# Kernel tuning notes

Hardware: AMD Instinct MI355X
Metric: run time of the kernel (lower is better)

The kernel has to match this reference:

```python
import jax, jax.numpy as jnp
import numpy as np
from jax import lax

B, N, NP, NS, CIN = 4, 8192, 2048, 32, 64
RADIUS = 0.1
CH = [CIN + 3, 64, 64, 128]  # mlp[0] += 3 because use_xyz=True
EPS = 1e-5


def _gather(x, idx):
    # x: [B, N, D], idx: [B, ...] int -> [B, ..., D]
    return jax.vmap(lambda a, i: a[i])(x, idx)


def _fps(xyz, npoint):
    # furthest point sampling, returns indices [B, npoint]
    b, n, _ = xyz.shape
    init_idx = jnp.zeros((b,), jnp.int32)
    dist0 = jnp.full((b, n), 1e10, xyz.dtype)

    def body(carry, _):
        dist, last = carry
        p = jnp.take_along_axis(xyz, last[:, None, None], axis=1)  # [B,1,3]
        d = jnp.sum((xyz - p) ** 2, axis=-1)                       # [B,N]
        dist = jnp.minimum(dist, d)
        nxt = jnp.argmax(dist, axis=-1).astype(jnp.int32)
        return (dist, nxt), nxt

    (_, _), rest = lax.scan(body, (dist0, init_idx), None, length=npoint - 1)
    return jnp.concatenate([init_idx[None, :], rest], axis=0).T    # [B, npoint]


def _ball_query(xyz, new_xyz, radius, nsample):
    # first `nsample` points within radius; pad with the first hit (0 if none)
    n = xyz.shape[1]
    d2 = jnp.sum((new_xyz[:, :, None, :] - xyz[:, None, :, :]) ** 2, axis=-1)  # [B,NP,N]
    score = jnp.where(d2 < radius * radius, jnp.arange(n, dtype=jnp.int32), n)
    neg_vals, _ = lax.top_k(-score, nsample)   # smallest indices first
    idx = -neg_vals                            # [B,NP,nsample]
    first = idx[..., :1]
    fill = jnp.where(first >= n, 0, first)
    return jnp.where(idx >= n, fill, idx)


def setup_inputs() -> dict:
    key = jax.random.key(0)
    ks = jax.random.split(key, 16)
    inp = {
        "xyz": jax.random.uniform(ks[0], (B, N, 3), jnp.float32),
        "features": jax.random.normal(ks[1], (B, CIN, N), jnp.float32),
    }
    for i in range(3):
        ci, co = CH[i], CH[i + 1]
        inp[f"W{i}"] = jax.random.normal(ks[2 + 4 * i], (co, ci), jnp.float32) / np.sqrt(ci)
        inp[f"b{i}"] = jnp.zeros((co,), jnp.float32)
        inp[f"g{i}"] = jnp.ones((co,), jnp.float32)
        inp[f"beta{i}"] = jnp.zeros((co,), jnp.float32)
    return inp


def _forward(xyz, features, params):
    fps_idx = _fps(xyz, NP)
    new_xyz = _gather(xyz, fps_idx)                                 # [B,NP,3]
    idx = _ball_query(xyz, new_xyz, RADIUS, NS)                     # [B,NP,NS]
    g_xyz = _gather(xyz, idx) - new_xyz[:, :, None, :]              # relative xyz
    g_feat = _gather(jnp.swapaxes(features, 1, 2), idx)             # [B,NP,NS,CIN]
    h = jnp.concatenate([g_xyz, g_feat], axis=-1)                   # [B,NP,NS,3+CIN]
    for (W, b, g, be) in params:
        h = jnp.einsum('bpsc,oc->bpso', h, W) + b                   # 1x1 conv
        mu = jnp.mean(h, axis=(0, 1, 2))
        var = jnp.var(h, axis=(0, 1, 2))
        h = (h - mu) * lax.rsqrt(var + EPS) * g + be                # BatchNorm2d (batch stats)
        h = jax.nn.relu(h)
    new_features = jnp.max(h, axis=2)                               # max-pool over nsample
    return new_xyz, jnp.swapaxes(new_features, 1, 2)                # [B,Cout,NP]


def reference(xyz, features, W0, b0, g0, beta0, W1, b1, g1, beta1, W2, b2, g2, beta2):
    params = ((W0, b0, g0, beta0), (W1, b1, g1, beta1), (W2, b2, g2, beta2))
    return _forward(xyz, features, params)
```

## Files before the change

### kernel.cpp

```cpp
#include <hip/hip_runtime.h>
#include <hip/hip_bf16.h>
#include <cstdint>

#define B_   4
#define N_   8192
#define NP_  2048
#define NS_  32
#define CIN_ 64
#define M_   (B_*NP_*NS_)
#define EPS_ 1e-5f
#define R2_  0.01f

typedef unsigned long long ull;
typedef float v2f __attribute__((ext_vector_type(2)));

__global__ __launch_bounds__(256) void transpose_kernel(const float* __restrict__ feat,
                                                        __hip_bfloat16* __restrict__ featT)
{
    __shared__ float tile[64][65];
    const int b  = blockIdx.y;
    const int j0 = blockIdx.x * 64;
    const int tx = threadIdx.x & 63, ty = threadIdx.x >> 6;
    for (int cc = ty; cc < 64; cc += 4)
        tile[tx][cc] = feat[((size_t)(b*CIN_ + cc))*N_ + j0 + tx];
    __syncthreads();
    for (int cc = ty; cc < 64; cc += 4)
        featT[((size_t)(b*N_ + j0 + cc))*64 + tx] = __float2bfloat16(tile[cc][tx]);
}

template<int CTRL>
__device__ __forceinline__ float dppmaxf(float v)
{
    int o = __builtin_amdgcn_update_dpp(__float_as_int(v), __float_as_int(v), CTRL, 0xF, 0xF, false);
    return fmaxf(v, __int_as_float(o));
}

__global__ __launch_bounds__(512) void fps_kernel(const float* __restrict__ xyz,
    int* __restrict__ fps_idx, float* __restrict__ new_xyzf, float* __restrict__ out)
{
#pragma clang fp contract(off)
    const int b = blockIdx.x;
    const int t = threadIdx.x;
    const float* X = xyz + (size_t)b * N_ * 3;

    __shared__ float xs[N_], ys[N_], zs[N_];
    __shared__ float wavemax[8];
    __shared__ unsigned widx_slot[2];

    for (int p = t; p < N_; p += 512) {
        xs[p] = X[p*3+0]; ys[p] = X[p*3+1]; zs[p] = X[p*3+2];
    }
    if (t < 2) widx_slot[t] = 0u;

    v2f px[8], py[8], pz[8], dst[8];
#pragma unroll
    for (int g = 0; g < 8; ++g) {
        const int p0 = (2*g)*512 + t, p1 = (2*g+1)*512 + t;
        px[g] = (v2f){X[p0*3+0], X[p1*3+0]};
        py[g] = (v2f){X[p0*3+1], X[p1*3+1]};
        pz[g] = (v2f){X[p0*3+2], X[p1*3+2]};
        dst[g] = (v2f){1e10f, 1e10f};
    }
    const int wv = t >> 6, ln = t & 63;

    float cx = X[0], cy = X[1], cz = X[2];
    if (t == 0) {
        fps_idx[b*NP_] = 0;
        size_t o3 = (size_t)(b*NP_) * 3;
        new_xyzf[o3] = cx; new_xyzf[o3+1] = cy; new_xyzf[o3+2] = cz;
        out[o3] = cx; out[o3+1] = cy; out[o3+2] = cz;
    }
    for (int it = 1; it < NP_; ++it) {
        const int par = it & 1;
        float bestv = -1.0f;
        const v2f c0 = (v2f){cx, cx}, c1 = (v2f){cy, cy}, c2 = (v2f){cz, cz};
#pragma unroll
        for (int g = 0; g < 8; ++g) {
            v2f dx = px[g] - c0, dy = py[g] - c1, dz = pz[g] - c2;
            v2f dd = dx*dx;
            dd = dd + dy*dy;
            dd = dd + dz*dz;
            v2f nd;
            nd.x = fminf(dst[g].x, dd.x);
            nd.y = fminf(dst[g].y, dd.y);
            dst[g] = nd;
            bestv = fmaxf(bestv, nd.x);
            bestv = fmaxf(bestv, nd.y);
        }
        float wm = bestv;
        wm = dppmaxf<0x111>(wm);
        wm = dppmaxf<0x112>(wm);
        wm = dppmaxf<0x114>(wm);
        wm = dppmaxf<0x118>(wm);
        wm = dppmaxf<0x142>(wm);
        wm = dppmaxf<0x143>(wm);
        if (ln == 63) wavemax[wv] = wm;
        __syncthreads();
        if (t == 0) widx_slot[par ^ 1] = 0u;
        float bmax = fmaxf(fmaxf(fmaxf(wavemax[0], wavemax[1]), fmaxf(wavemax[2], wavemax[3])),
                           fmaxf(fmaxf(wavemax[4], wavemax[5]), fmaxf(wavemax[6], wavemax[7])));
        if (bestv == bmax) {
            unsigned nin = 0u;
#pragma unroll
            for (int g = 7; g >= 0; --g) {
                if (dst[g].y == bmax) nin = ~(unsigned)((2*g+1)*512 + t);
                if (dst[g].x == bmax) nin = ~(unsigned)((2*g)*512 + t);
            }
            atomicMax(&widx_slot[par], nin);
        }
        __syncthreads();
        const int widx = (int)(~widx_slot[par]);
        cx = xs[widx]; cy = ys[widx]; cz = zs[widx];
        if (t == 0) {
            fps_idx[b*NP_ + it] = widx;
            size_t o3 = ((size_t)(b*NP_ + it)) * 3;
            new_xyzf[o3] = cx; new_xyzf[o3+1] = cy; new_xyzf[o3+2] = cz;
            out[o3] = cx; out[o3+1] = cy; out[o3+2] = cz;
        }
    }
}

__global__ __launch_bounds__(256) void ball_kernel(const float* __restrict__ xyz,
    const float* __restrict__ new_xyzf, int* __restrict__ ballidx)
{
#pragma clang fp contract(off)
    const int gw   = (blockIdx.x * 256 + threadIdx.x) >> 6;
    const int lane = threadIdx.x & 63;
    const int b    = gw >> 11;
    const float* X = xyz + (size_t)b * N_ * 3;
    const float cx = new_xyzf[(size_t)gw*3];
    const float cy = new_xyzf[(size_t)gw*3+1];
    const float cz = new_xyzf[(size_t)gw*3+2];
    int* outp = ballidx + (size_t)gw * NS_;
    int total = 0, first = -1;
    for (int base = 0; base < N_; base += 64) {
        const int j = base + lane;
        float dx = cx - X[j*3], dy = cy - X[j*3+1], dz = cz - X[j*3+2];
        float d2 = dx*dx;
        d2 = d2 + dy*dy;
        d2 = d2 + dz*dz;
        const bool in = d2 <= R2_;
        ull m = __ballot(in);
        if (m) {
            if (first < 0) first = base + __builtin_ctzll(m);
            int r = total + __popcll(m & ((1ull << lane) - 1ull));
            if (in && r < NS_) outp[r] = j;
            total += (int)__popcll(m);
            if (total >= NS_) break;
        }
    }
    if (total < NS_) {
        int f = first < 0 ? 0 : first;
        if (lane >= total && lane < NS_) outp[lane] = f;
    }
}

__global__ __launch_bounds__(256) void gemm1_kernel(const float* __restrict__ xyz,
    const __hip_bfloat16* __restrict__ featT, const float* __restrict__ newxyz,
    const int* __restrict__ ballidx, const float* __restrict__ W, const float* __restrict__ bias,
    __hip_bfloat16* __restrict__ pre1, float* __restrict__ psum, float* __restrict__ psumsq)
{
    const int lane = threadIdx.x & 63;
    const int gw   = (blockIdx.x * 256 + threadIdx.x) >> 6;
    float w[67];
#pragma unroll
    for (int k = 0; k < 67; ++k) w[k] = W[lane*67 + k];
    const float bs = bias[lane];
    float s1 = 0.f, s2 = 0.f;
    for (int r = gw; r < M_; r += 4096) {
        const int b = r >> 16;
        const int p = (r & 65535) >> 5;
        const int j = ballidx[r];
        const float* xp = xyz    + ((size_t)b*N_  + j)*3;
        const float* cp = newxyz + ((size_t)b*NP_ + p)*3;
        float acc = bs;
        acc = fmaf(xp[0] - cp[0], w[0], acc);
        acc = fmaf(xp[1] - cp[1], w[1], acc);
        acc = fmaf(xp[2] - cp[2], w[2], acc);
        const unsigned* rp = (const unsigned*)(featT + ((size_t)b*N_ + j)*64);
#pragma unroll
        for (int kk = 0; kk < 32; ++kk) {
            unsigned u = rp[kk];
            float v0 = __uint_as_float(u << 16);
            float v1 = __uint_as_float(u & 0xffff0000u);
            acc = fmaf(v0, w[3 + 2*kk], acc);
            acc = fmaf(v1, w[4 + 2*kk], acc);
        }
        pre1[(size_t)r*64 + lane] = __float2bfloat16(acc);
        s1 += acc;
        s2 = fmaf(acc, acc, s2);
    }
    psum  [(size_t)gw*64 + lane] = s1;
    psumsq[(size_t)gw*64 + lane] = s2;
}

__global__ __launch_bounds__(256) void gemm2_kernel(__hip_bfloat16* __restrict__ buf,
    const float* __restrict__ W, const float* __restrict__ bias,
    const float* __restrict__ bnsc, const float* __restrict__ bnsh,
    float* __restrict__ psum, float* __restrict__ psumsq)
{
    const int lane = threadIdx.x & 63;
    const int gw   = (blockIdx.x * 256 + threadIdx.x) >> 6;
    __shared__ float ssc[64], ssh[64];
    if (threadIdx.x < 64) { ssc[threadIdx.x] = bnsc[threadIdx.x]; ssh[threadIdx.x] = bnsh[threadIdx.x]; }
    __syncthreads();
    float w[64];
#pragma unroll
    for (int k = 0; k < 64; ++k) w[k] = W[lane*64 + k];
    const float bs = bias[lane];
    float s1 = 0.f, s2 = 0.f;
    for (int r = gw; r < M_; r += 4096) {
        const unsigned* rp = (const unsigned*)(buf + (size_t)r*64);
        float acc = bs;
#pragma unroll
        for (int kk = 0; kk < 32; ++kk) {
            unsigned u = rp[kk];
            float v0 = __uint_as_float(u << 16);
            float v1 = __uint_as_float(u & 0xffff0000u);
            v0 = fmaxf(fmaf(v0, ssc[2*kk],   ssh[2*kk]),   0.f);
            v1 = fmaxf(fmaf(v1, ssc[2*kk+1], ssh[2*kk+1]), 0.f);
            acc = fmaf(v0, w[2*kk],   acc);
            acc = fmaf(v1, w[2*kk+1], acc);
        }
        buf[(size_t)r*64 + lane] = __float2bfloat16(acc);
        s1 += acc;
        s2 = fmaf(acc, acc, s2);
    }
    psum  [(size_t)gw*64 + lane] = s1;
    psumsq[(size_t)gw*64 + lane] = s2;
}

__global__ __launch_bounds__(256) void gemm3_kernel(const __hip_bfloat16* __restrict__ pre2,
    const float* __restrict__ W, const float* __restrict__ bias,
    const float* __restrict__ bnsc, const float* __restrict__ bnsh,
    float* __restrict__ mxb, float* __restrict__ mnb,
    float* __restrict__ psum, float* __restrict__ psumsq)
{
    const int lane = threadIdx.x & 63;
    const int gw   = (blockIdx.x * 256 + threadIdx.x) >> 6;
    const int pt   = gw >> 1;
    const int half = gw & 1;
    __shared__ float ssc[64], ssh[64];
    if (threadIdx.x < 64) { ssc[threadIdx.x] = bnsc[threadIdx.x]; ssh[threadIdx.x] = bnsh[threadIdx.x]; }
    __syncthreads();
    const int o = half*64 + lane;
    float w[64];
#pragma unroll
    for (int k = 0; k < 64; ++k) w[k] = W[o*64 + k];
    const float bs = bias[o];
    float s1 = 0.f, s2 = 0.f, mx = -1e30f, mn = 1e30f;
    for (int s = 0; s < NS_; ++s) {
        const size_t r = (size_t)pt*NS_ + s;
        const unsigned* rp = (const unsigned*)(pre2 + r*64);
        float acc = bs;
#pragma unroll
        for (int kk = 0; kk < 32; ++kk) {
            unsigned u = rp[kk];
            float v0 = __uint_as_float(u << 16);
            float v1 = __uint_as_float(u & 0xffff0000u);
            v0 = fmaxf(fmaf(v0, ssc[2*kk],   ssh[2*kk]),   0.f);
            v1 = fmaxf(fmaf(v1, ssc[2*kk+1], ssh[2*kk+1]), 0.f);
            acc = fmaf(v0, w[2*kk],   acc);
            acc = fmaf(v1, w[2*kk+1], acc);
        }
        s1 += acc;
        s2 = fmaf(acc, acc, s2);
        mx = fmaxf(mx, acc);
        mn = fminf(mn, acc);
    }
    mxb[(size_t)pt*128 + o] = mx;
    mnb[(size_t)pt*128 + o] = mn;
    psum  [(size_t)pt*128 + o] = s1;
    psumsq[(size_t)pt*128 + o] = s2;
}

template<int CO>
__global__ __launch_bounds__(256) void bnred_kernel(const float* __restrict__ psum,
    const float* __restrict__ psumsq, const float* __restrict__ g, const float* __restrict__ beta,
    float* __restrict__ sc, float* __restrict__ sh, int nslots)
{
    const int c = blockIdx.x;
    const int t = threadIdx.x;
    float s1 = 0, s2 = 0;
    for (int i = t; i < nslots; i += 256) {
        s1 += psum  [(size_t)i*CO + c];
        s2 += psumsq[(size_t)i*CO + c];
    }
    __shared__ float a1[256], a2[256];
    a1[t] = s1; a2[t] = s2;
    __syncthreads();
    for (int st = 128; st > 0; st >>= 1) {
        if (t < st) { a1[t] += a1[t+st]; a2[t] += a2[t+st]; }
        __syncthreads();
    }
    if (t == 0) {
        const float invM = 1.0f / (float)M_;
        float mu  = a1[0] * invM;
        float var = fmaxf(a2[0] * invM - mu*mu, 0.f);
        float rs  = 1.0f / sqrtf(var + EPS_);
        float s   = rs * g[c];
        sc[c] = s;
        sh[c] = fmaf(-mu, s, beta[c]);
    }
}

__global__ __launch_bounds__(256) void final_kernel(const float* __restrict__ mxb,
    const float* __restrict__ mnb, const float* __restrict__ sc, const float* __restrict__ sh,
    float* __restrict__ out)
{
    __shared__ float tile[128][65];
    const int b = blockIdx.y, p0 = blockIdx.x * 64;
    {
        const int o = threadIdx.x & 127, ph = threadIdx.x >> 7;
        const float s = sc[o], h = sh[o];
        const bool pos = (s >= 0.f);
        for (int pl = ph; pl < 64; pl += 2) {
            const size_t pt = (size_t)b*NP_ + p0 + pl;
            float v = pos ? mxb[pt*128 + o] : mnb[pt*128 + o];
            tile[o][pl] = fmaxf(fmaf(v, s, h), 0.f);
        }
    }
    __syncthreads();
    {
        const int p = threadIdx.x & 63, oh = threadIdx.x >> 6;
        for (int oo = oh; oo < 128; oo += 4)
            out[(size_t)(B_*NP_*3) + ((size_t)(b*128 + oo))*NP_ + p0 + p] = tile[oo][p];
    }
}

extern "C" void kernel_launch(void* const* d_in, const int* in_sizes, int n_in,
                              void* d_out, int out_size, void* d_ws, size_t ws_size,
                              hipStream_t stream)
{
    const float* xyz  = (const float*)d_in[0];
    const float* feat = (const float*)d_in[1];
    const float* W0   = (const float*)d_in[2];
    const float* b0   = (const float*)d_in[3];
    const float* g0   = (const float*)d_in[4];
    const float* be0  = (const float*)d_in[5];
    const float* W1   = (const float*)d_in[6];
    const float* b1   = (const float*)d_in[7];
    const float* g1   = (const float*)d_in[8];
    const float* be1  = (const float*)d_in[9];
    const float* W2   = (const float*)d_in[10];
    const float* b2   = (const float*)d_in[11];
    const float* g2   = (const float*)d_in[12];
    const float* be2  = (const float*)d_in[13];

    char* ws = (char*)d_ws;
    int*   fpsidx = (int*)  (ws + 0);
    float* newxyz = (float*)(ws + 32768);
    int*   ball   = (int*)  (ws + 131072);
    float* scb    = (float*)(ws + 1179648);
    float* psum   = (float*)(ws + 1183744);
    float* psumsq = (float*)(ws + 5378048);
    __hip_bfloat16* featT = (__hip_bfloat16*)(ws + 9572352);
    float* mxb    = (float*)(ws + 13766656);
    float* mnb    = (float*)(ws + 17960960);
    __hip_bfloat16* buf1 = (__hip_bfloat16*)(ws + 22155264);
    float* out = (float*)d_out;

    float* sc1 = scb;       float* sh1 = scb + 128;
    float* sc2 = scb + 256; float* sh2 = scb + 384;
    float* sc3 = scb + 512; float* sh3 = scb + 640;

    transpose_kernel<<<dim3(N_/64, B_), 256, 0, stream>>>(feat, featT);
    fps_kernel<<<dim3(B_), 512, 0, stream>>>(xyz, fpsidx, newxyz, out);
    ball_kernel<<<dim3(B_*NP_/4), 256, 0, stream>>>(xyz, newxyz, ball);

    gemm1_kernel<<<1024, 256, 0, stream>>>(xyz, featT, newxyz, ball, W0, b0, buf1, psum, psumsq);
    bnred_kernel<64><<<64, 256, 0, stream>>>(psum, psumsq, g0, be0, sc1, sh1, 4096);
    gemm2_kernel<<<1024, 256, 0, stream>>>(buf1, W1, b1, sc1, sh1, psum, psumsq);
    bnred_kernel<64><<<64, 256, 0, stream>>>(psum, psumsq, g1, be1, sc2, sh2, 4096);
    gemm3_kernel<<<4096, 256, 0, stream>>>(buf1, W2, b2, sc2, sh2, mxb, mnb, psum, psumsq);
    bnred_kernel<128><<<128, 256, 0, stream>>>(psum, psumsq, g2, be2, sc3, sh3, 8192);
    final_kernel<<<dim3(NP_/64, B_), 256, 0, stream>>>(mxb, mnb, sc3, sh3, out);
}
```

Baseline: 2.545 ms.

## Pick FPS winner via wave ballot and pass coordinates through shared slot

Each thread now owns a contiguous block of 16 points instead of a 512-strided set. With that layout, the lowest-index winner is found by taking the lowest wave whose maximum matches, then the lowest lane in a ballot, with no shared-memory atomicMax. The winning thread writes its own register coordinates into a small shared slot. This removes the 96KB shared xyz copy and the atomic. The risk is that the contiguous per-thread layout makes the initial global loads uncoalesced, though those run only once.

Result: slower. 2.790 ms (+9.7%).

```diff
diff --git a/kernel.cpp b/kernel.cpp
--- a/kernel.cpp
+++ b/kernel.cpp
@@ -43,19 +43,14 @@
     const int t = threadIdx.x;
     const float* X = xyz + (size_t)b * N_ * 3;
 
-    __shared__ float xs[N_], ys[N_], zs[N_];
     __shared__ float wavemax[8];
-    __shared__ unsigned widx_slot[2];
-
-    for (int p = t; p < N_; p += 512) {
-        xs[p] = X[p*3+0]; ys[p] = X[p*3+1]; zs[p] = X[p*3+2];
-    }
-    if (t < 2) widx_slot[t] = 0u;
+    __shared__ float slot[3];
+    __shared__ int   slotidx;
 
     v2f px[8], py[8], pz[8], dst[8];
 #pragma unroll
     for (int g = 0; g < 8; ++g) {
-        const int p0 = (2*g)*512 + t, p1 = (2*g+1)*512 + t;
+        const int p0 = t*16 + 2*g, p1 = p0 + 1;
         px[g] = (v2f){X[p0*3+0], X[p1*3+0]};
         py[g] = (v2f){X[p0*3+1], X[p1*3+1]};
         pz[g] = (v2f){X[p0*3+2], X[p1*3+2]};
@@ -71,7 +66,6 @@
         out[o3] = cx; out[o3+1] = cy; out[o3+2] = cz;
     }
     for (int it = 1; it < NP_; ++it) {
-        const int par = it & 1;
         float bestv = -1.0f;
         const v2f c0 = (v2f){cx, cx}, c1 = (v2f){cy, cy}, c2 = (v2f){cz, cz};
 #pragma unroll
@@ -96,22 +90,36 @@
         wm = dppmaxf<0x143>(wm);
         if (ln == 63) wavemax[wv] = wm;
         __syncthreads();
-        if (t == 0) widx_slot[par ^ 1] = 0u;
-        float bmax = fmaxf(fmaxf(fmaxf(wavemax[0], wavemax[1]), fmaxf(wavemax[2], wavemax[3])),
-                           fmaxf(fmaxf(wavemax[4], wavemax[5]), fmaxf(wavemax[6], wavemax[7])));
-        if (bestv == bmax) {
-            unsigned nin = 0u;
-#pragma unroll
-            for (int g = 7; g >= 0; --g) {
-                if (dst[g].y == bmax) nin = ~(unsigned)((2*g+1)*512 + t);
-                if (dst[g].x == bmax) nin = ~(unsigned)((2*g)*512 + t);
+        const float v0 = wavemax[0], v1 = wavemax[1], v2 = wavemax[2], v3 = wavemax[3];
+        const float v4 = wavemax[4], v5 = wavemax[5], v6 = wavemax[6], v7 = wavemax[7];
+        const float bmax = fmaxf(fmaxf(fmaxf(v0, v1), fmaxf(v2, v3)),
+                                 fmaxf(fmaxf(v4, v5), fmaxf(v6, v7)));
+        int wstar = 7;
+        if (v6 == bmax) wstar = 6;
+        if (v5 == bmax) wstar = 5;
+        if (v4 == bmax) wstar = 4;
+        if (v3 == bmax) wstar = 3;
+        if (v2 == bmax) wstar = 2;
+        if (v1 == bmax) wstar = 1;
+        if (v0 == bmax) wstar = 0;
+        if (wv == wstar) {
+            const ull mask = __ballot(bestv == bmax);
+            const int lstar = __builtin_ctzll(mask);
+            if (ln == lstar) {
+                int jj = 0; float wx = 0.f, wy = 0.f, wz = 0.f;
+#pragma unroll
+                for (int g = 7; g >= 0; --g) {
+                    if (dst[g].y == bmax) { jj = 2*g+1; wx = px[g].y; wy = py[g].y; wz = pz[g].y; }
+                    if (dst[g].x == bmax) { jj = 2*g;   wx = px[g].x; wy = py[g].x; wz = pz[g].x; }
+                }
+                slot[0] = wx; slot[1] = wy; slot[2] = wz;
+                slotidx = t*16 + jj;
             }
-            atomicMax(&widx_slot[par], nin);
         }
         __syncthreads();
-        const int widx = (int)(~widx_slot[par]);
-        cx = xs[widx]; cy = ys[widx]; cz = zs[widx];
+        cx = slot[0]; cy = slot[1]; cz = slot[2];
         if (t == 0) {
+            const int widx = slotidx;
             fps_idx[b*NP_ + it] = widx;
             size_t o3 = ((size_t)(b*NP_ + it)) * 3;
             new_xyzf[o3] = cx; new_xyzf[o3+1] = cy; new_xyzf[o3+2] = cz;
```

## Cut FPS argmax to one barrier using per-wave packed max/index slots

Applied to the files above, without the earlier changes.

Each FPS iteration now finds the wave-local max distance and the matching smallest index entirely with DPP reductions plus readlane. Each wave writes a packed (value, index) 64-bit slot to double-buffered shared memory, and every thread reduces the eight slots after a single barrier. This removes the second __syncthreads, the shared-memory atomicMax and the slot reset from a loop that runs 2047 times serially. The cost is extra DPP work per iteration, since every wave now does the index reduction instead of only the lanes holding the block max. The per-thread max is also split into two independent chains for more ILP.

New measurement: 2.742 ms. +7.8%, slower.

```diff
diff --git a/kernel.cpp b/kernel.cpp
--- a/kernel.cpp
+++ b/kernel.cpp
@@ -34,6 +34,12 @@
     int o = __builtin_amdgcn_update_dpp(__float_as_int(v), __float_as_int(v), CTRL, 0xF, 0xF, false);
     return fmaxf(v, __int_as_float(o));
 }
+template<int CTRL>
+__device__ __forceinline__ unsigned dppmaxu(unsigned v)
+{
+    unsigned o = (unsigned)__builtin_amdgcn_update_dpp((int)v, (int)v, CTRL, 0xF, 0xF, false);
+    return v > o ? v : o;
+}
 
 __global__ __launch_bounds__(512) void fps_kernel(const float* __restrict__ xyz,
     int* __restrict__ fps_idx, float* __restrict__ new_xyzf, float* __restrict__ out)
@@ -44,14 +50,11 @@
     const float* X = xyz + (size_t)b * N_ * 3;
 
     __shared__ float xs[N_], ys[N_], zs[N_];
-    __shared__ float wavemax[8];
-    __shared__ unsigned widx_slot[2];
+    __shared__ ull slots[2][8];
 
     for (int p = t; p < N_; p += 512) {
         xs[p] = X[p*3+0]; ys[p] = X[p*3+1]; zs[p] = X[p*3+2];
     }
-    if (t < 2) widx_slot[t] = 0u;
-
     v2f px[8], py[8], pz[8], dst[8];
 #pragma unroll
     for (int g = 0; g < 8; ++g) {
@@ -70,9 +73,10 @@
         new_xyzf[o3] = cx; new_xyzf[o3+1] = cy; new_xyzf[o3+2] = cz;
         out[o3] = cx; out[o3+1] = cy; out[o3+2] = cz;
     }
+    __syncthreads();
     for (int it = 1; it < NP_; ++it) {
         const int par = it & 1;
-        float bestv = -1.0f;
+        v2f bm = (v2f){-1.0f, -1.0f};
         const v2f c0 = (v2f){cx, cx}, c1 = (v2f){cy, cy}, c2 = (v2f){cz, cz};
 #pragma unroll
         for (int g = 0; g < 8; ++g) {
@@ -84,9 +88,10 @@
             nd.x = fminf(dst[g].x, dd.x);
             nd.y = fminf(dst[g].y, dd.y);
             dst[g] = nd;
-            bestv = fmaxf(bestv, nd.x);
-            bestv = fmaxf(bestv, nd.y);
-        }
+            bm.x = fmaxf(bm.x, nd.x);
+            bm.y = fmaxf(bm.y, nd.y);
+        }
+        const float bestv = fmaxf(bm.x, bm.y);
         float wm = bestv;
         wm = dppmaxf<0x111>(wm);
         wm = dppmaxf<0x112>(wm);
@@ -94,22 +99,44 @@
         wm = dppmaxf<0x118>(wm);
         wm = dppmaxf<0x142>(wm);
         wm = dppmaxf<0x143>(wm);
-        if (ln == 63) wavemax[wv] = wm;
+        const float wm_b = __int_as_float(__builtin_amdgcn_readlane(__float_as_int(wm), 63));
+        unsigned nin = 0u;
+        if (bestv == wm_b) {
+#pragma unroll
+            for (int g = 7; g >= 0; --g) {
+                if (dst[g].y == wm_b) nin = ~(unsigned)((2*g+1)*512 + t);
+                if (dst[g].x == wm_b) nin = ~(unsigned)((2*g)*512 + t);
+            }
+        }
+        nin = dppmaxu<0x111>(nin);
+        nin = dppmaxu<0x112>(nin);
+        nin = dppmaxu<0x114>(nin);
+        nin = dppmaxu<0x118>(nin);
+        nin = dppmaxu<0x142>(nin);
+        nin = dppmaxu<0x143>(nin);
+        if (ln == 63) slots[par][wv] = ((ull)__float_as_uint(wm_b) << 32) | nin;
         __syncthreads();
-        if (t == 0) widx_slot[par ^ 1] = 0u;
-        float bmax = fmaxf(fmaxf(fmaxf(wavemax[0], wavemax[1]), fmaxf(wavemax[2], wavemax[3])),
-                           fmaxf(fmaxf(wavemax[4], wavemax[5]), fmaxf(wavemax[6], wavemax[7])));
-        if (bestv == bmax) {
-            unsigned nin = 0u;
-#pragma unroll
-            for (int g = 7; g >= 0; --g) {
-                if (dst[g].y == bmax) nin = ~(unsigned)((2*g+1)*512 + t);
-                if (dst[g].x == bmax) nin = ~(unsigned)((2*g)*512 + t);
-            }
-            atomicMax(&widx_slot[par], nin);
-        }
-        __syncthreads();
-        const int widx = (int)(~widx_slot[par]);
+        const ull s0 = slots[par][0], s1 = slots[par][1], s2 = slots[par][2], s3 = slots[par][3];
+        const ull s4 = slots[par][4], s5 = slots[par][5], s6 = slots[par][6], s7 = slots[par][7];
+        const float w0 = __uint_as_float((unsigned)(s0 >> 32)), w1 = __uint_as_float((unsigned)(s1 >> 32));
+        const float w2 = __uint_as_float((unsigned)(s2 >> 32)), w3 = __uint_as_float((unsigned)(s3 >> 32));
+        const float w4 = __uint_as_float((unsigned)(s4 >> 32)), w5 = __uint_as_float((unsigned)(s5 >> 32));
+        const float w6 = __uint_as_float((unsigned)(s6 >> 32)), w7 = __uint_as_float((unsigned)(s7 >> 32));
+        const float bmax = fmaxf(fmaxf(fmaxf(w0, w1), fmaxf(w2, w3)),
+                                 fmaxf(fmaxf(w4, w5), fmaxf(w6, w7)));
+        unsigned m0 = (w0 == bmax) ? (unsigned)s0 : 0u;
+        unsigned m1 = (w1 == bmax) ? (unsigned)s1 : 0u;
+        unsigned m2 = (w2 == bmax) ? (unsigned)s2 : 0u;
+        unsigned m3 = (w3 == bmax) ? (unsigned)s3 : 0u;
+        unsigned m4 = (w4 == bmax) ? (unsigned)s4 : 0u;
+        unsigned m5 = (w5 == bmax) ? (unsigned)s5 : 0u;
+        unsigned m6 = (w6 == bmax) ? (unsigned)s6 : 0u;
+        unsigned m7 = (w7 == bmax) ? (unsigned)s7 : 0u;
+        m0 = m0 > m1 ? m0 : m1;  m2 = m2 > m3 ? m2 : m3;
+        m4 = m4 > m5 ? m4 : m5;  m6 = m6 > m7 ? m6 : m7;
+        m0 = m0 > m2 ? m0 : m2;  m4 = m4 > m6 ? m4 : m6;
+        const unsigned nsel = m0 > m4 ? m0 : m4;
+        const int widx = (int)(~nsel);
         cx = xs[widx]; cy = ys[widx]; cz = zs[widx];
         if (t == 0) {
             fps_idx[b*NP_ + it] = widx;
```

## Split BN+ReLU into separate elementwise pass and vectorize GEMM row loads

Applied to the files above, without the earlier changes.

BatchNorm scale/shift and ReLU move out of the inner loops of gemm2 and gemm3 into a standalone epi_kernel. That kernel rewrites the bf16 activation buffer in place before each GEMM. All three GEMM kernels now read each 64-channel bf16 row as 16-byte uint4 loads instead of 32 scalar 4-byte loads. This removes per-element FMA/max work and shared-memory lookups that every output lane repeated. The cost is two extra full read/write passes over the 64 MB activation buffer, plus bf16 rounding after the BN/ReLU step.

Result: faster. 2.381 ms (-6.4%).

```diff
diff --git a/kernel.cpp b/kernel.cpp
--- a/kernel.cpp
+++ b/kernel.cpp
@@ -177,14 +177,19 @@
         acc = fmaf(xp[0] - cp[0], w[0], acc);
         acc = fmaf(xp[1] - cp[1], w[1], acc);
         acc = fmaf(xp[2] - cp[2], w[2], acc);
-        const unsigned* rp = (const unsigned*)(featT + ((size_t)b*N_ + j)*64);
-#pragma unroll
-        for (int kk = 0; kk < 32; ++kk) {
-            unsigned u = rp[kk];
-            float v0 = __uint_as_float(u << 16);
-            float v1 = __uint_as_float(u & 0xffff0000u);
-            acc = fmaf(v0, w[3 + 2*kk], acc);
-            acc = fmaf(v1, w[4 + 2*kk], acc);
+        const uint4* rp = (const uint4*)(featT + ((size_t)b*N_ + j)*64);
+#pragma unroll
+        for (int q = 0; q < 8; ++q) {
+            const uint4 u4 = rp[q];
+            const unsigned uu0 = u4.x, uu1 = u4.y, uu2 = u4.z, uu3 = u4.w;
+            acc = fmaf(__uint_as_float(uu0 << 16),         w[3 + q*8 + 0], acc);
+            acc = fmaf(__uint_as_float(uu0 & 0xffff0000u), w[3 + q*8 + 1], acc);
+            acc = fmaf(__uint_as_float(uu1 << 16),         w[3 + q*8 + 2], acc);
+            acc = fmaf(__uint_as_float(uu1 & 0xffff0000u), w[3 + q*8 + 3], acc);
+            acc = fmaf(__uint_as_float(uu2 << 16),         w[3 + q*8 + 4], acc);
+            acc = fmaf(__uint_as_float(uu2 & 0xffff0000u), w[3 + q*8 + 5], acc);
+            acc = fmaf(__uint_as_float(uu3 << 16),         w[3 + q*8 + 6], acc);
+            acc = fmaf(__uint_as_float(uu3 & 0xffff0000u), w[3 + q*8 + 7], acc);
         }
         pre1[(size_t)r*64 + lane] = __float2bfloat16(acc);
         s1 += acc;
@@ -194,33 +199,60 @@
     psumsq[(size_t)gw*64 + lane] = s2;
 }
 
+__global__ __launch_bounds__(256) void epi_kernel(__hip_bfloat16* __restrict__ buf,
+    const float* __restrict__ sc, const float* __restrict__ sh)
+{
+    __shared__ float ssc[64], ssh[64];
+    if (threadIdx.x < 64) { ssc[threadIdx.x] = sc[threadIdx.x]; ssh[threadIdx.x] = sh[threadIdx.x]; }
+    __syncthreads();
+    const size_t idx = (size_t)blockIdx.x * 256 + threadIdx.x;
+    const int k0 = (threadIdx.x & 7) * 8;
+    uint4* p = (uint4*)buf;
+    uint4 u = p[idx];
+    unsigned wds[4] = {u.x, u.y, u.z, u.w};
+    unsigned res[4];
+#pragma unroll
+    for (int m = 0; m < 4; ++m) {
+        const int k = k0 + m*2;
+        float v0 = __uint_as_float(wds[m] << 16);
+        float v1 = __uint_as_float(wds[m] & 0xffff0000u);
+        v0 = fmaxf(fmaf(v0, ssc[k],   ssh[k]),   0.f);
+        v1 = fmaxf(fmaf(v1, ssc[k+1], ssh[k+1]), 0.f);
+        __hip_bfloat16 b0 = __float2bfloat16(v0);
+        __hip_bfloat16 b1 = __float2bfloat16(v1);
+        unsigned short s0 = *reinterpret_cast<unsigned short*>(&b0);
+        unsigned short s1 = *reinterpret_cast<unsigned short*>(&b1);
+        res[m] = (unsigned)s0 | ((unsigned)s1 << 16);
+    }
+    p[idx] = make_uint4(res[0], res[1], res[2], res[3]);
+}
+
 __global__ __launch_bounds__(256) void gemm2_kernel(__hip_bfloat16* __restrict__ buf,
     const float* __restrict__ W, const float* __restrict__ bias,
-    const float* __restrict__ bnsc, const float* __restrict__ bnsh,
     float* __restrict__ psum, float* __restrict__ psumsq)
 {
     const int lane = threadIdx.x & 63;
     const int gw   = (blockIdx.x * 256 + threadIdx.x) >> 6;
-    __shared__ float ssc[64], ssh[64];
-    if (threadIdx.x < 64) { ssc[threadIdx.x] = bnsc[threadIdx.x]; ssh[threadIdx.x] = bnsh[threadIdx.x]; }
-    __syncthreads();
     float w[64];
 #pragma unroll
     for (int k = 0; k < 64; ++k) w[k] = W[lane*64 + k];
     const float bs = bias[lane];
     float s1 = 0.f, s2 = 0.f;
     for (int r = gw; r < M_; r += 4096) {
-        const unsigned* rp = (const unsigned*)(buf + (size_t)r*64);
+        const uint4* rp = (const uint4*)(buf + (size_t)r*64);
         float acc = bs;
 #pragma unroll
-        for (int kk = 0; kk < 32; ++kk) {
-            unsigned u = rp[kk];
-            float v0 = __uint_as_float(u << 16);
-            float v1 = __uint_as_float(u & 0xffff0000u);
-            v0 = fmaxf(fmaf(v0, ssc[2*kk],   ssh[2*kk]),   0.f);
-            v1 = fmaxf(fmaf(v1, ssc[2*kk+1], ssh[2*kk+1]), 0.f);
-            acc = fmaf(v0, w[2*kk],   acc);
-            acc = fmaf(v1, w[2*kk+1], acc);
+        for (int q = 0; q < 8; ++q) {
+            const uint4 u4 = rp[q];
+            const unsigned uu0 = u4.x, uu1 = u4.y, uu2 = u4.z, uu3 = u4.w;
+            acc = fmaf(__uint_as_float(uu0 << 16),         w[q*8 + 0], acc);
+            acc = fmaf(__uint_as_float(uu0 & 0xffff0000u), w[q*8 + 1], acc);
+            acc = fmaf(__uint_as_float(uu1 << 16),         w[q*8 + 2], acc);
+            acc = fmaf(__uint_as_float(uu1 & 0xffff0000u), w[q*8 + 3], acc);
+            acc = fmaf(__uint_as_float(uu2 << 16),         w[q*8 + 4], acc);
+            acc = fmaf(__uint_as_float(uu2 & 0xffff0000u), w[q*8 + 5], acc);
+            acc = fmaf(__uint_as_float(uu3 << 16),         w[q*8 + 6], acc);
+            acc = fmaf(__uint_as_float(uu3 & 0xffff0000u), w[q*8 + 7], acc);
         }
         buf[(size_t)r*64 + lane] = __float2bfloat16(acc);
         s1 += acc;
@@ -230,9 +262,8 @@
     psumsq[(size_t)gw*64 + lane] = s2;
 }
 
-__global__ __launch_bounds__(256) void gemm3_kernel(const __hip_bfloat16* __restrict__ pre2,
+__global__ __launch_bounds__(256) void gemm3_kernel(const __hip_bfloat16* __restrict__ act2,
     const float* __restrict__ W, const float* __restrict__ bias,
-    const float* __restrict__ bnsc, const float* __restrict__ bnsh,
     float* __restrict__ mxb, float* __restrict__ mnb,
     float* __restrict__ psum, float* __restrict__ psumsq)
 {
@@ -240,9 +271,6 @@
     const int gw   = (blockIdx.x * 256 + threadIdx.x) >> 6;
     const int pt   = gw >> 1;
     const int half = gw & 1;
-    __shared__ float ssc[64], ssh[64];
-    if (threadIdx.x < 64) { ssc[threadIdx.x] = bnsc[threadIdx.x]; ssh[threadIdx.x] = bnsh[threadIdx.x]; }
-    __syncthreads();
     const int o = half*64 + lane;
     float w[64];
 #pragma unroll
@@ -251,17 +279,20 @@
     float s1 = 0.f, s2 = 0.f, mx = -1e30f, mn = 1e30f;
     for (int s = 0; s < NS_; ++s) {
         const size_t r = (size_t)pt*NS_ + s;
-        const unsigned* rp = (const unsigned*)(pre2 + r*64);
+        const uint4* rp = (const uint4*)(act2 + r*64);
         float acc = bs;
 #pragma unroll
-        for (int kk = 0; kk < 32; ++kk) {
-            unsigned u = rp[kk];
-            float v0 = __uint_as_float(u << 16);
-            float v1 = __uint_as_float(u & 0xffff0000u);
-            v0 = fmaxf(fmaf(v0, ssc[2*kk],   ssh[2*kk]),   0.f);
-            v1 = fmaxf(fmaf(v1, ssc[2*kk+1], ssh[2*kk+1]), 0.f);
-            acc = fmaf(v0, w[2*kk],   acc);
-            acc = fmaf(v1, w[2*kk+1], acc);
+        for (int q = 0; q < 8; ++q) {
+            const uint4 u4 = rp[q];
+            const unsigned uu0 = u4.x, uu1 = u4.y, uu2 = u4.z, uu3 = u4.w;
+            acc = fmaf(__uint_as_float(uu0 << 16),         w[q*8 + 0], acc);
+            acc = fmaf(__uint_as_float(uu0 & 0xffff0000u), w[q*8 + 1], acc);
+            acc = fmaf(__uint_as_float(uu1 << 16),         w[q*8 + 2], acc);
+            acc = fmaf(__uint_as_float(uu1 & 0xffff0000u), w[q*8 + 3], acc);
+            acc = fmaf(__uint_as_float(uu2 << 16),         w[q*8 + 4], acc);
+            acc = fmaf(__uint_as_float(uu2 & 0xffff0000u), w[q*8 + 5], acc);
+            acc = fmaf(__uint_as_float(uu3 << 16),         w[q*8 + 6], acc);
+            acc = fmaf(__uint_as_float(uu3 & 0xffff0000u), w[q*8 + 7], acc);
         }
         s1 += acc;
         s2 = fmaf(acc, acc, s2);
@@ -370,9 +401,11 @@
 
     gemm1_kernel<<<1024, 256, 0, stream>>>(xyz, featT, newxyz, ball, W0, b0, buf1, psum, psumsq);
     bnred_kernel<64><<<64, 256, 0, stream>>>(psum, psumsq, g0, be0, sc1, sh1, 4096);
-    gemm2_kernel<<<1024, 256, 0, stream>>>(buf1, W1, b1, sc1, sh1, psum, psumsq);
+    epi_kernel<<<M_*64/8/256, 256, 0, stream>>>(buf1, sc1, sh1);
+    gemm2_kernel<<<1024, 256, 0, stream>>>(buf1, W1, b1, psum, psumsq);
     bnred_kernel<64><<<64, 256, 0, stream>>>(psum, psumsq, g1, be1, sc2, sh2, 4096);
-    gemm3_kernel<<<4096, 256, 0, stream>>>(buf1, W2, b2, sc2, sh2, mxb, mnb, psum, psumsq);
+    epi_kernel<<<M_*64/8/256, 256, 0, stream>>>(buf1, sc2, sh2);
+    gemm3_kernel<<<4096, 256, 0, stream>>>(buf1, W2, b2, mxb, mnb, psum, psumsq);
     bnred_kernel<128><<<128, 256, 0, stream>>>(psum, psumsq, g2, be2, sc3, sh3, 8192);
     final_kernel<<<dim3(NP_/64, B_), 256, 0, stream>>>(mxb, mnb, sc3, sh3, out);
 }
```
